# Kernel optimization log

Measured on AMD Instinct MI355X. Metric: run time of the kernel, lower is better.

## Reference

```python
import jax, jax.numpy as jnp
import numpy as np

B, K, F, INCH, OUTCH, R = 16, 8, 512, 512, 512, 8


def setup_inputs() -> dict:
    key = jax.random.key(0)
    ks = jax.random.split(key, 10)
    inp = {
        "x": jax.random.normal(ks[0], (B, K, F, INCH), jnp.float32),
        "u": jax.random.normal(ks[1], (B, K, OUTCH, R), jnp.float32),
        "v": jax.random.normal(ks[2], (B, K, INCH, R), jnp.float32),
        "b": jax.random.normal(ks[3], (B, 1, 1, OUTCH), jnp.float32) * 0.02,
        # learned parameters (torch nn.Linear layout: W [out, in])
        "W_pass": jax.random.normal(ks[4], (INCH // 2, INCH), jnp.float32) * 0.02,
        "b_pass": jax.random.normal(ks[5], (INCH // 2,), jnp.float32) * 0.02,
        "W_ave": jax.random.normal(ks[6], (INCH // 2, INCH), jnp.float32) * 0.02,
        "b_ave": jax.random.normal(ks[7], (INCH // 2,), jnp.float32) * 0.02,
        "W_out": jax.random.normal(ks[8], (OUTCH, INCH), jnp.float32) * 0.02,
        "b_out": jax.random.normal(ks[9], (OUTCH,), jnp.float32) * 0.02,
    }
    return inp


def reference(x, u, v, b, W_pass, b_pass, W_ave, b_ave, W_out, b_out):
    # x: [B,K,F,inch]
    k = x.shape[1]
    # 'ave' branch: linear -> mean over K -> broadcast back to K
    y = jnp.einsum('bkfi,hi->bkfh', x, W_ave) + b_ave        # [B,K,F,inch//2]
    y = jnp.broadcast_to(jnp.mean(y, axis=1, keepdims=True), y.shape)
    # 'pass' branch
    xp = jnp.einsum('bkfi,hi->bkfh', x, W_pass) + b_pass      # [B,K,F,inch//2]
    h = jnp.concatenate([xp, y], axis=-1)                     # [B,K,F,inch]
    h = jax.nn.gelu(h, approximate=False)                     # dropout is identity in eval
    # LoRA term: mean(v * h) over inch, then mean(u * z) over R
    inch = h.shape[-1]
    r = v.shape[-1]
    z = jnp.einsum('bkfi,bkir->bkfr', h, v) / inch            # [B,K,F,R]
    lora = jnp.einsum('bkfr,bkor->bkfo', z, u) / r            # [B,K,F,outch]
    out = jnp.einsum('bkfi,oi->bkfo', h, W_out) + b_out + lora + b
    out = jax.nn.gelu(out, approximate=False)
    return out
```

## Files before the change

kernel.cpp:

```cpp
#include <hip/hip_runtime.h>
#include <stdint.h>


typedef __attribute__((ext_vector_type(8))) __bf16 bf16x8;
typedef __attribute__((ext_vector_type(4))) float f32x4;
typedef __attribute__((ext_vector_type(8))) unsigned short ushort8;
typedef __attribute__((ext_vector_type(4))) unsigned short ushort4_t;
typedef __attribute__((ext_vector_type(4))) float float4_t;

#define MFMA16(a, b, c) __builtin_amdgcn_mfma_f32_16x16x32_bf16((a), (b), (c), 0, 0, 0)
#define GLL16(g, l)                                                                   \
    __builtin_amdgcn_global_load_lds((const __attribute__((address_space(1))) void*)(g), \
                                     (__attribute__((address_space(3))) void*)(l), 16, 0, 0)

__device__ inline unsigned short f2bf(float f) {
    union { float fv; unsigned u; } un; un.fv = f;
    unsigned u = un.u;
    u += 0x7FFFu + ((u >> 16) & 1u);
    return (unsigned short)(u >> 16);
}

__device__ inline float geluf(float x) {
    float x2 = x * x;
    float inner = x + 0.044715f * x * x2;
    float e = __expf(-1.5957691216057308f * inner);
    return x * __builtin_amdgcn_rcpf(1.0f + e);
}

__device__ inline bf16x8 lds8(const unsigned short* p) {
    return __builtin_bit_cast(bf16x8, *(const ushort8*)p);
}

__device__ inline void stage_w(const unsigned short* __restrict__ src, long rowbase,
                               long stride, int k0, unsigned short* buf, int l) {
#pragma unroll
    for (int it = 0; it < 4; ++it) {
        const int s = it * 64 + l;
        const int r = s >> 2;
        const int j = (s & 3) ^ (r & 3);
        GLL16(src + (rowbase + r) * stride + k0 + j * 8, &buf[it * 512]);
    }
}

__device__ inline bf16x8 ldw(const unsigned short* buf, int rbase, int l) {
    const int r = rbase + (l & 15);
    const int j = l >> 4;
    return lds8(&buf[r * 32 + (((j ^ r) & 3) << 3)]);
}

__global__ void cvt_all(const float* __restrict__ a, const float* __restrict__ b,
                        const float* __restrict__ c, unsigned short* __restrict__ oa,
                        unsigned short* __restrict__ ob, unsigned short* __restrict__ oc) {
    int bid = blockIdx.x;
    const float* s; unsigned short* d; int off;
    if (bid < 128) { s = a; d = oa; off = bid; }
    else if (bid < 256) { s = b; d = ob; off = bid - 128; }
    else { s = c; d = oc; off = bid - 256; }
    int i = off * 256 + threadIdx.x;
    float4_t v = *(const float4_t*)(s + (size_t)i * 4);
    ushort4_t r;
    r[0] = f2bf(v[0]); r[1] = f2bf(v[1]); r[2] = f2bf(v[2]); r[3] = f2bf(v[3]);
    *(ushort4_t*)(d + (size_t)i * 4) = r;
}

__global__ void mean_cvt(const float* __restrict__ x,
                         unsigned short* __restrict__ xb,
                         unsigned short* __restrict__ xm) {
    int gid = blockIdx.x * 256 + threadIdx.x;
    int c  = gid & 127;
    int bf = gid >> 7;
    int b  = bf >> 9;
    int f  = bf & 511;
    float4_t s = {0.f, 0.f, 0.f, 0.f};
#pragma unroll
    for (int k = 0; k < 8; ++k) {
        long row = (long)(b * 8 + k) * 512 + f;
        float4_t v = *(const float4_t*)(x + row * 512 + c * 4);
        s += v;
        ushort4_t t;
        t[0] = f2bf(v[0]); t[1] = f2bf(v[1]); t[2] = f2bf(v[2]); t[3] = f2bf(v[3]);
        *(ushort4_t*)(xb + row * 512 + c * 4) = t;
    }
    ushort4_t t;
    t[0] = f2bf(s[0] * 0.125f); t[1] = f2bf(s[1] * 0.125f);
    t[2] = f2bf(s[2] * 0.125f); t[3] = f2bf(s[3] * 0.125f);
    *(ushort4_t*)(xm + (long)bf * 512 + c * 4) = t;
}

__launch_bounds__(256)
__global__ void gemm_gelu(const unsigned short* __restrict__ A,
                          const unsigned short* __restrict__ W,
                          const float* __restrict__ bias,
                          unsigned short* __restrict__ O,
                          int chunk) {
    __shared__ __align__(16) unsigned short S[32768];
    const int tid = threadIdx.x;
    const int w = tid >> 6, l = tid & 63;
    const int wr = w >> 1, wc = w & 1;
    const int work = ((blockIdx.x & 7) * chunk) + (blockIdx.x >> 3);
    const int nt = work & 1;
    const int mt = work >> 1;
    const long row0 = (long)mt * 128 + wr * 64;
    const long col0 = (long)nt * 128 + wc * 64;

    unsigned short* aw[2] = { &S[w * 4096],        &S[16384 + w * 4096] };
    unsigned short* bw[2] = { &S[w * 4096 + 2048], &S[16384 + w * 4096 + 2048] };

    f32x4 acc[4][4];
    const f32x4 z4 = {0.f, 0.f, 0.f, 0.f};
#pragma unroll
    for (int i = 0; i < 4; ++i)
#pragma unroll
        for (int j = 0; j < 4; ++j) acc[i][j] = z4;

    stage_w(A, row0, 512, 0, aw[0], l);
    stage_w(W, col0, 512, 0, bw[0], l);

#pragma unroll
    for (int t = 0; t < 16; ++t) {
        if (t < 15) {
            stage_w(A, row0, 512, (t + 1) * 32, aw[(t + 1) & 1], l);
            stage_w(W, col0, 512, (t + 1) * 32, bw[(t + 1) & 1], l);
            asm volatile("s_waitcnt vmcnt(8)" ::: "memory");
        } else {
            asm volatile("s_waitcnt vmcnt(0)" ::: "memory");
        }
        const unsigned short* ab = aw[t & 1];
        const unsigned short* bb = bw[t & 1];
        bf16x8 af[4], bfr[4];
#pragma unroll
        for (int mi = 0; mi < 4; ++mi) af[mi] = ldw(ab, mi * 16, l);
#pragma unroll
        for (int nj = 0; nj < 4; ++nj) bfr[nj] = ldw(bb, nj * 16, l);
        __builtin_amdgcn_s_setprio(1);
#pragma unroll
        for (int mi = 0; mi < 4; ++mi)
#pragma unroll
            for (int nj = 0; nj < 4; ++nj)
                acc[mi][nj] = MFMA16(af[mi], bfr[nj], acc[mi][nj]);
        __builtin_amdgcn_s_setprio(0);
    }

#pragma unroll
    for (int mi = 0; mi < 4; ++mi) {
        const long rb = row0 + mi * 16 + (l >> 4) * 4;
#pragma unroll
        for (int nj = 0; nj < 4; ++nj) {
            const long cg = col0 + nj * 16 + (l & 15);
            const float bv = bias[cg];
#pragma unroll
            for (int q = 0; q < 4; ++q)
                O[(rb + q) * 256 + cg] = f2bf(geluf(acc[mi][nj][q] + bv));
        }
    }
}

__launch_bounds__(256)
__global__ void zcalc_s(const unsigned short* __restrict__ Hp,
                        const unsigned short* __restrict__ Gy,
                        const float* __restrict__ v,
                        unsigned short* __restrict__ zb) {
    __shared__ __align__(16) unsigned short Vt[16 * 536];
    const int tid = threadIdx.x;
    const int w = tid >> 6, l = tid & 63;
    const int mt = blockIdx.x;
    const long row0 = (long)mt * 128;
    const int gb = (mt >> 5) * 512 + (mt & 3) * 128;
    {
        ushort8 zz = {0, 0, 0, 0, 0, 0, 0, 0};
        for (int i = tid; i < (16 * 536) / 8; i += 256) *(ushort8*)&Vt[i * 8] = zz;
        __syncthreads();
        const float* vp = v + (long)(mt >> 2) * 4096;
#pragma unroll
        for (int p = 0; p < 4; ++p) {
            float4_t vv = *(const float4_t*)(vp + tid * 16 + p * 4);
#pragma unroll
            for (int j = 0; j < 4; ++j) {
                int flat = tid * 16 + p * 4 + j;
                Vt[(flat & 7) * 536 + (flat >> 3)] = f2bf(vv[j] * (1.0f / 512.0f));
            }
        }
        __syncthreads();
    }
    const unsigned short* ph[2];
    const unsigned short* pg[2];
#pragma unroll
    for (int q = 0; q < 2; ++q) {
        const int r = (w * 2 + q) * 16 + (l & 15);
        ph[q] = Hp + (row0 + r) * 256 + (l >> 4) * 8;
        pg[q] = Gy + (size_t)(gb + r) * 256 + (l >> 4) * 8;
    }
    f32x4 zacc[2];
    const f32x4 z4 = {0.f, 0.f, 0.f, 0.f};
    zacc[0] = z4; zacc[1] = z4;
#pragma unroll
    for (int ks = 0; ks < 8; ++ks) {
        bf16x8 bv = lds8(&Vt[(l & 15) * 536 + ks * 32 + (l >> 4) * 8]);
#pragma unroll
        for (int q = 0; q < 2; ++q)
            zacc[q] = MFMA16(lds8(ph[q] + ks * 32), bv, zacc[q]);
    }
#pragma unroll
    for (int ks = 0; ks < 8; ++ks) {
        bf16x8 bv = lds8(&Vt[(l & 15) * 536 + 256 + ks * 32 + (l >> 4) * 8]);
#pragma unroll
        for (int q = 0; q < 2; ++q)
            zacc[q] = MFMA16(lds8(pg[q] + ks * 32), bv, zacc[q]);
    }
    if ((l & 15) < 8) {
#pragma unroll
        for (int q = 0; q < 2; ++q) {
            const int fr = w * 2 + q;
#pragma unroll
            for (int reg = 0; reg < 4; ++reg) {
                long r = row0 + fr * 16 + (l >> 4) * 4 + reg;
                zb[r * 8 + (l & 15)] = f2bf(zacc[q][reg]);
            }
        }
    }
}

__launch_bounds__(256)
__global__ void gemm_out(const unsigned short* __restrict__ Hp,
                         const unsigned short* __restrict__ Gy,
                         const unsigned short* __restrict__ Wo,
                         const float* __restrict__ bo,
                         const float* __restrict__ bb,
                         const float* __restrict__ u,
                         const unsigned short* __restrict__ zb,
                         float* __restrict__ Out) {
    __shared__ __align__(16) unsigned short S[32768];
    const int tid = threadIdx.x;
    const int w = tid >> 6, l = tid & 63;
    const int wr = w >> 1, wc = w & 1;
    const int work = ((blockIdx.x & 7) * 256) + (blockIdx.x >> 3);
    const int nt = work & 3;
    const int mt = work >> 2;
    const long row0 = (long)mt * 128;
    const long arow = row0 + wr * 64;
    const long grow = (long)((mt >> 5) * 512 + (mt & 3) * 128) + wr * 64;
    const long col0 = (long)nt * 128 + wc * 64;
    const int bk = mt >> 2;
    const int bi = bk >> 3;

    unsigned short* aw[2] = { &S[w * 4096],        &S[16384 + w * 4096] };
    unsigned short* bw[2] = { &S[w * 4096 + 2048], &S[16384 + w * 4096 + 2048] };

    f32x4 acc[4][4];
    const f32x4 z4 = {0.f, 0.f, 0.f, 0.f};
#pragma unroll
    for (int i = 0; i < 4; ++i)
#pragma unroll
        for (int j = 0; j < 4; ++j) acc[i][j] = z4;

    stage_w(Hp, arow, 256, 0, aw[0], l);
    stage_w(Wo, col0, 512, 0, bw[0], l);

#pragma unroll
    for (int t = 0; t < 16; ++t) {
        if (t < 15) {
            const int tt = t + 1;
            if (tt < 8) stage_w(Hp, arow, 256, tt * 32, aw[tt & 1], l);
            else        stage_w(Gy, grow, 256, (tt - 8) * 32, aw[tt & 1], l);
            stage_w(Wo, col0, 512, tt * 32, bw[tt & 1], l);
            asm volatile("s_waitcnt vmcnt(8)" ::: "memory");
        } else {
            asm volatile("s_waitcnt vmcnt(0)" ::: "memory");
        }
        const unsigned short* ab = aw[t & 1];
        const unsigned short* bbuf = bw[t & 1];
        bf16x8 af[4], bfr[4];
#pragma unroll
        for (int mi = 0; mi < 4; ++mi) af[mi] = ldw(ab, mi * 16, l);
#pragma unroll
        for (int nj = 0; nj < 4; ++nj) bfr[nj] = ldw(bbuf, nj * 16, l);
        __builtin_amdgcn_s_setprio(1);
#pragma unroll
        for (int mi = 0; mi < 4; ++mi)
#pragma unroll
            for (int nj = 0; nj < 4; ++nj)
                acc[mi][nj] = MFMA16(af[mi], bfr[nj], acc[mi][nj]);
        __builtin_amdgcn_s_setprio(0);
    }

    __syncthreads();
    {
        ushort8 zz = {0, 0, 0, 0, 0, 0, 0, 0};
        const int row = tid >> 1;
        if ((tid & 1) == 0) {
            *(ushort8*)&S[row * 32]     = *(const ushort8*)&zb[(row0 + row) * 8];
            *(ushort8*)&S[row * 32 + 8] = zz;
        } else {
            *(ushort8*)&S[row * 32 + 16] = zz;
            *(ushort8*)&S[row * 32 + 24] = zz;
        }
    }
    __syncthreads();

    const float* up = u + (long)bk * 4096;
#pragma unroll
    for (int nj = 0; nj < 4; ++nj) {
        const long og = col0 + nj * 16 + (l & 15);
        ushort8 ubits = {0, 0, 0, 0, 0, 0, 0, 0};
        if ((l >> 4) == 0) {
            float4_t u0 = *(const float4_t*)(up + og * 8);
            float4_t u1 = *(const float4_t*)(up + og * 8 + 4);
            ubits[0] = f2bf(u0[0] * 0.125f); ubits[1] = f2bf(u0[1] * 0.125f);
            ubits[2] = f2bf(u0[2] * 0.125f); ubits[3] = f2bf(u0[3] * 0.125f);
            ubits[4] = f2bf(u1[0] * 0.125f); ubits[5] = f2bf(u1[1] * 0.125f);
            ubits[6] = f2bf(u1[2] * 0.125f); ubits[7] = f2bf(u1[3] * 0.125f);
        }
        bf16x8 ub = __builtin_bit_cast(bf16x8, ubits);
#pragma unroll
        for (int mi = 0; mi < 4; ++mi) {
            bf16x8 az = lds8(&S[(wr * 64 + mi * 16 + (l & 15)) * 32 + (l >> 4) * 8]);
            acc[mi][nj] = MFMA16(az, ub, acc[mi][nj]);
        }
    }

#pragma unroll
    for (int mi = 0; mi < 4; ++mi) {
        const long rb = row0 + wr * 64 + mi * 16 + (l >> 4) * 4;
#pragma unroll
        for (int nj = 0; nj < 4; ++nj) {
            const long og = col0 + nj * 16 + (l & 15);
            const float badd = bo[og] + bb[bi * 512 + og];
#pragma unroll
            for (int q = 0; q < 4; ++q)
                Out[(rb + q) * 512 + og] = geluf(acc[mi][nj][q] + badd);
        }
    }
}

extern "C" void kernel_launch(void* const* d_in, const int* in_sizes, int n_in,
                              void* d_out, int out_size, void* d_ws, size_t ws_size,
                              hipStream_t stream) {
    const float* x  = (const float*)d_in[0];
    const float* u  = (const float*)d_in[1];
    const float* v  = (const float*)d_in[2];
    const float* bb = (const float*)d_in[3];
    const float* Wp = (const float*)d_in[4];
    const float* bp = (const float*)d_in[5];
    const float* Wa = (const float*)d_in[6];
    const float* ba = (const float*)d_in[7];
    const float* Wo = (const float*)d_in[8];
    const float* bo = (const float*)d_in[9];
    float* out = (float*)d_out;

    char* ws = (char*)d_ws;
    unsigned short* xb  = (unsigned short*)(ws + 0);
    unsigned short* zb  = (unsigned short*)(ws + 0);
    unsigned short* xm  = (unsigned short*)(ws + 67108864);
    unsigned short* gy  = (unsigned short*)(ws + 75497472);
    unsigned short* hp  = (unsigned short*)(ws + 79691776);
    unsigned short* Wpb = (unsigned short*)(ws + 113246208);
    unsigned short* Wab = (unsigned short*)(ws + 113508352);
    unsigned short* Wob = (unsigned short*)(ws + 113770496);

    cvt_all<<<512, 256, 0, stream>>>(Wp, Wa, Wo, Wpb, Wab, Wob);
    mean_cvt<<<4096, 256, 0, stream>>>(x, xb, xm);
    gemm_gelu<<<128, 256, 0, stream>>>(xm, Wab, ba, gy, 16);
    gemm_gelu<<<1024, 256, 0, stream>>>(xb, Wpb, bp, hp, 128);
    zcalc_s<<<512, 256, 0, stream>>>(hp, gy, v, zb);
    gemm_out<<<2048, 256, 0, stream>>>(hp, gy, Wob, bo, bb, u, zb, out);
}
```

Before: 170.7 us.

## Stage GEMM epilogues through LDS for coalesced stores, widen mean_cvt vectors

After: 169.0 us. No clear change (-1.0%).

```diff
diff --git a/kernel.cpp b/kernel.cpp
--- a/kernel.cpp
+++ b/kernel.cpp
@@ -67,24 +67,29 @@
                          unsigned short* __restrict__ xb,
                          unsigned short* __restrict__ xm) {
     int gid = blockIdx.x * 256 + threadIdx.x;
-    int c  = gid & 127;
-    int bf = gid >> 7;
+    int c  = gid & 63;
+    int bf = gid >> 6;
     int b  = bf >> 9;
     int f  = bf & 511;
-    float4_t s = {0.f, 0.f, 0.f, 0.f};
+    float s0 = 0.f, s1 = 0.f, s2 = 0.f, s3 = 0.f, s4 = 0.f, s5 = 0.f, s6 = 0.f, s7 = 0.f;
 #pragma unroll
     for (int k = 0; k < 8; ++k) {
         long row = (long)(b * 8 + k) * 512 + f;
-        float4_t v = *(const float4_t*)(x + row * 512 + c * 4);
-        s += v;
-        ushort4_t t;
-        t[0] = f2bf(v[0]); t[1] = f2bf(v[1]); t[2] = f2bf(v[2]); t[3] = f2bf(v[3]);
-        *(ushort4_t*)(xb + row * 512 + c * 4) = t;
-    }
-    ushort4_t t;
-    t[0] = f2bf(s[0] * 0.125f); t[1] = f2bf(s[1] * 0.125f);
-    t[2] = f2bf(s[2] * 0.125f); t[3] = f2bf(s[3] * 0.125f);
-    *(ushort4_t*)(xm + (long)bf * 512 + c * 4) = t;
+        float4_t lo = *(const float4_t*)(x + row * 512 + c * 8);
+        float4_t hi = *(const float4_t*)(x + row * 512 + c * 8 + 4);
+        s0 += lo[0]; s1 += lo[1]; s2 += lo[2]; s3 += lo[3];
+        s4 += hi[0]; s5 += hi[1]; s6 += hi[2]; s7 += hi[3];
+        ushort8 t;
+        t[0] = f2bf(lo[0]); t[1] = f2bf(lo[1]); t[2] = f2bf(lo[2]); t[3] = f2bf(lo[3]);
+        t[4] = f2bf(hi[0]); t[5] = f2bf(hi[1]); t[6] = f2bf(hi[2]); t[7] = f2bf(hi[3]);
+        *(ushort8*)(xb + row * 512 + c * 8) = t;
+    }
+    ushort8 m;
+    m[0] = f2bf(s0 * 0.125f); m[1] = f2bf(s1 * 0.125f);
+    m[2] = f2bf(s2 * 0.125f); m[3] = f2bf(s3 * 0.125f);
+    m[4] = f2bf(s4 * 0.125f); m[5] = f2bf(s5 * 0.125f);
+    m[6] = f2bf(s6 * 0.125f); m[7] = f2bf(s7 * 0.125f);
+    *(ushort8*)(xm + (long)bf * 512 + c * 8) = m;
 }
 
 __launch_bounds__(256)
@@ -141,17 +146,29 @@
         __builtin_amdgcn_s_setprio(0);
     }
 
+    __syncthreads();
 #pragma unroll
     for (int mi = 0; mi < 4; ++mi) {
-        const long rb = row0 + mi * 16 + (l >> 4) * 4;
+        const int R0 = wr * 64 + mi * 16 + (l >> 4) * 4;
 #pragma unroll
         for (int nj = 0; nj < 4; ++nj) {
-            const long cg = col0 + nj * 16 + (l & 15);
-            const float bv = bias[cg];
+            const int C = wc * 64 + nj * 16 + (l & 15);
+            const float bv = bias[((col0 & ~63L) - wc * 64) + C];
 #pragma unroll
             for (int q = 0; q < 4; ++q)
-                O[(rb + q) * 256 + cg] = f2bf(geluf(acc[mi][nj][q] + bv));
-        }
+                S[(R0 + q) * 136 + C] = f2bf(geluf(acc[mi][nj][q] + bv));
+        }
+    }
+    __syncthreads();
+    const long rowt = (long)mt * 128;
+    const long colt = (long)nt * 128;
+#pragma unroll
+    for (int s = 0; s < 8; ++s) {
+        const int flat = s * 2048 + tid * 8;
+        const int row = flat >> 7;
+        const int col = flat & 127;
+        ushort8 vv = *(const ushort8*)&S[row * 136 + col];
+        *(ushort8*)(O + (rowt + row) * 256 + colt + col) = vv;
     }
 }
 
@@ -229,7 +246,9 @@
                          const float* __restrict__ u,
                          const unsigned short* __restrict__ zb,
                          float* __restrict__ Out) {
-    __shared__ __align__(16) unsigned short S[32768];
+    __shared__ __align__(16) char SM[67584];
+    unsigned short* S = (unsigned short*)SM;
+    float* Sf = (float*)SM;
     const int tid = threadIdx.x;
     const int w = tid >> 6, l = tid & 63;
     const int wr = w >> 1, wc = w & 1;
@@ -318,17 +337,29 @@
         }
     }
 
-#pragma unroll
-    for (int mi = 0; mi < 4; ++mi) {
-        const long rb = row0 + wr * 64 + mi * 16 + (l >> 4) * 4;
-#pragma unroll
-        for (int nj = 0; nj < 4; ++nj) {
-            const long og = col0 + nj * 16 + (l & 15);
-            const float badd = bo[og] + bb[bi * 512 + og];
+    __syncthreads();
+#pragma unroll
+    for (int nj = 0; nj < 4; ++nj) {
+        const long og = col0 + nj * 16 + (l & 15);
+        const float badd = bo[og] + bb[bi * 512 + og];
+        const int C = wc * 64 + nj * 16 + (l & 15);
+#pragma unroll
+        for (int mi = 0; mi < 4; ++mi) {
+            const int R0 = wr * 64 + mi * 16 + (l >> 4) * 4;
 #pragma unroll
             for (int q = 0; q < 4; ++q)
-                Out[(rb + q) * 512 + og] = geluf(acc[mi][nj][q] + badd);
-        }
+                Sf[(R0 + q) * 132 + C] = geluf(acc[mi][nj][q] + badd);
+        }
+    }
+    __syncthreads();
+    const long colt = (long)nt * 128;
+#pragma unroll
+    for (int s = 0; s < 16; ++s) {
+        const int flat = s * 1024 + tid * 4;
+        const int row = flat >> 7;
+        const int col = flat & 127;
+        float4_t vv = *(const float4_t*)&Sf[row * 132 + col];
+        __builtin_nontemporal_store(vv, (float4_t*)(Out + (row0 + row) * 512 + colt + col));
     }
 }
 
@@ -358,7 +389,7 @@
     unsigned short* Wob = (unsigned short*)(ws + 113770496);
 
     cvt_all<<<512, 256, 0, stream>>>(Wp, Wa, Wo, Wpb, Wab, Wob);
-    mean_cvt<<<4096, 256, 0, stream>>>(x, xb, xm);
+    mean_cvt<<<2048, 256, 0, stream>>>(x, xb, xm);
     gemm_gelu<<<128, 256, 0, stream>>>(xm, Wab, ba, gy, 16);
     gemm_gelu<<<1024, 256, 0, stream>>>(xb, Wpb, bp, hp, 128);
     zcalc_s<<<512, 256, 0, stream>>>(hp, gy, v, zb);
```
